# Kernel tuning notes

Measured on AMD Instinct MI355X. Metric: run time of the kernel, lower is better.

## Reference

```python
import jax, jax.numpy as jnp
import numpy as np

NHID = 512
NCLS = 250
CHUNK = 200  # words per class (equal class_chunks), vocab = NCLS*CHUNK = 50000
N = 2048     # flattened tokens (batch*seq after masking)


def setup_inputs() -> dict:
    key = jax.random.key(0)
    k1, k2, k3, k4, k5 = jax.random.split(key, 5)
    r = 0.1  # init_weights uniform range
    x = jax.random.normal(k1, (N, NHID), dtype=jnp.float32)
    cls_idx = jax.random.randint(k2, (N,), 0, NCLS, dtype=jnp.int64)
    Wc = jax.random.uniform(k3, (NCLS, NHID), jnp.float32, -r, r)   # cls_decoder.weight
    bc = jnp.zeros((NCLS,), jnp.float32)                             # cls_decoder.bias
    Ww = jax.random.uniform(k4, (NCLS, CHUNK, NHID), jnp.float32, -r, r)  # stacked words_decoders weights
    bw = jnp.zeros((NCLS, CHUNK), jnp.float32)                       # stacked words_decoders biases
    return {"x": x, "Wc": Wc, "bc": bc, "Ww": Ww, "bw": bw, "cls_idx": cls_idx}


def reference(x, Wc, bc, Ww, bw, cls_idx):
    # Class logits for every token: cls_decoder(input)
    p_class = jnp.einsum('nh,ch->nc', x, Wc) + bc          # [N, NCLS]
    # Per-class word decoders: each token goes through the Linear of its class.
    # Equivalent to the dict-based index_select + per-class Linear in the
    # original forward (rows reordered per-token instead of grouped by class).
    Wg = Ww[cls_idx]                                       # [N, CHUNK, NHID] irregular gather
    bg = bw[cls_idx]                                       # [N, CHUNK]
    p_words = jnp.einsum('nkh,nh->nk', Wg, x) + bg         # [N, CHUNK]
    # Concatenate class and within-class logits into one array output.
    return jnp.concatenate([p_class, p_words], axis=1)     # [N, NCLS+CHUNK]
```

## Files before the change

### kernel.cpp

```cpp
#include <hip/hip_runtime.h>

#define NHID   512
#define NCLS   250
#define CHUNK  200
#define NTOK   2048
#define NOUT   450
#define NBLK   500
#define NTHR   256
#define MAXTOK 64

typedef __attribute__((ext_vector_type(8))) short bf16x8;
typedef __attribute__((ext_vector_type(4))) float f32x4;

#define MFMA(a, b, c) __builtin_amdgcn_mfma_f32_16x16x32_bf16((a), (b), (c), 0, 0, 0)

__device__ __forceinline__ unsigned hpack(unsigned a, unsigned b) {
    return __builtin_amdgcn_perm(a, b, 0x07060302u);
}

__device__ __forceinline__ void cvt8(f32x4 va, f32x4 vb, bf16x8& h, bf16x8& l) {
    unsigned u0 = __float_as_uint(va[0]), u1 = __float_as_uint(va[1]);
    unsigned u2 = __float_as_uint(va[2]), u3 = __float_as_uint(va[3]);
    unsigned u4 = __float_as_uint(vb[0]), u5 = __float_as_uint(vb[1]);
    unsigned u6 = __float_as_uint(vb[2]), u7 = __float_as_uint(vb[3]);
    union { unsigned w[4]; bf16x8 v; } H, L;
    H.w[0] = hpack(u1, u0); H.w[1] = hpack(u3, u2);
    H.w[2] = hpack(u5, u4); H.w[3] = hpack(u7, u6);
    float r0 = va[0] - __uint_as_float(u0 & 0xffff0000u);
    float r1 = va[1] - __uint_as_float(u1 & 0xffff0000u);
    float r2 = va[2] - __uint_as_float(u2 & 0xffff0000u);
    float r3 = va[3] - __uint_as_float(u3 & 0xffff0000u);
    float r4 = vb[0] - __uint_as_float(u4 & 0xffff0000u);
    float r5 = vb[1] - __uint_as_float(u5 & 0xffff0000u);
    float r6 = vb[2] - __uint_as_float(u6 & 0xffff0000u);
    float r7 = vb[3] - __uint_as_float(u7 & 0xffff0000u);
    L.w[0] = hpack(__float_as_uint(r1), __float_as_uint(r0));
    L.w[1] = hpack(__float_as_uint(r3), __float_as_uint(r2));
    L.w[2] = hpack(__float_as_uint(r5), __float_as_uint(r4));
    L.w[3] = hpack(__float_as_uint(r7), __float_as_uint(r6));
    h = H.v; l = L.v;
}

#define WAITVM(nn) asm volatile("s_waitcnt vmcnt(" #nn ")" ::: "memory")
#define BL(k, off) asm volatile("global_load_dwordx4 %0, %1, off offset:%c2" \
        : "=v"(bv[k]) : "v"(wrow8), "i"(off))
#define BL2(s) BL(2*(s), (s)*128); BL(2*(s)+1, (s)*128 + 16)

#define KSTEP(s) { \
    const char* ab_ = (const char*)Afrag + n * 2048 + (s) * 128; \
    bf16x8 ah_ = *(const bf16x8*)(ab_ + (((q*2    ) ^ (n&7)) << 4)); \
    bf16x8 al_ = *(const bf16x8*)(ab_ + (((q*2 + 1) ^ (n&7)) << 4)); \
    bf16x8 bh_, bl_; cvt8(bv[2*(s)], bv[2*(s)+1], bh_, bl_); \
    acc = MFMA(ah_, bh_, acc); \
    acc = MFMA(al_, bh_, acc); \
    acc = MFMA(ah_, bl_, acc); }

__device__ __forceinline__ void class_unit(int u, int w8, int lane, int n, int q,
                                           const float* __restrict__ x,
                                           const float* __restrict__ Wc,
                                           const float* __restrict__ bc,
                                           float* __restrict__ out) {
    const int mt = u >> 1, hn = u & 1;
    const int g4 = (w8 >> 2) & 1, kk = w8 & 3;
    const int rC = (hn * 8 + g4 * 4 + kk) * 16 + n;
    const bool rv = rC < NCLS;
    const int  rc = rv ? rC : NCLS - 1;
    const float* ap = x  + (size_t)(mt * 16 + n) * NHID + q * 8;
    const float* bp = Wc + (size_t)rc * NHID + q * 8;
    const float bias = bc[rc];
    f32x4 acc = {0.f, 0.f, 0.f, 0.f};
    f32x4 qa[2][2], qb[2][2];
    #pragma unroll
    for (int j = 0; j < 2; ++j) {
        qa[j][0] = *(const f32x4*)(ap + j * 32);
        qa[j][1] = *(const f32x4*)(ap + j * 32 + 4);
        qb[j][0] = *(const f32x4*)(bp + j * 32);
        qb[j][1] = *(const f32x4*)(bp + j * 32 + 4);
    }
    #pragma unroll 2
    for (int s = 0; s < 16; ++s) {
        const int b = s & 1;
        bf16x8 ah, al, bh, bl;
        cvt8(qa[b][0], qa[b][1], ah, al);
        cvt8(qb[b][0], qb[b][1], bh, bl);
        acc = MFMA(ah, bh, acc);
        acc = MFMA(al, bh, acc);
        acc = MFMA(ah, bl, acc);
        if (s + 2 < 16) {
            qa[b][0] = *(const f32x4*)(ap + (s + 2) * 32);
            qa[b][1] = *(const f32x4*)(ap + (s + 2) * 32 + 4);
            qb[b][0] = *(const f32x4*)(bp + (s + 2) * 32);
            qb[b][1] = *(const f32x4*)(bp + (s + 2) * 32 + 4);
        }
    }
    if (rv) {
        #pragma unroll
        for (int i = 0; i < 4; ++i)
            out[(size_t)(mt * 16 + q * 4 + i) * NOUT + rc] = acc[i] + bias;
    }
}

__global__ __launch_bounds__(NTHR, 2)
void cbd_fused(const float* __restrict__ x,  const float* __restrict__ Wc,
               const float* __restrict__ bc, const float* __restrict__ Ww,
               const float* __restrict__ bw, const int* __restrict__ cls_idx,
               float* __restrict__ out)
{
    __shared__ short Afrag[16384];
    __shared__ int   toktmp[MAXTOK];

    const int tid  = threadIdx.x;
    const int wid  = tid >> 6;
    const int lane = tid & 63;
    const int n    = lane & 15;
    const int q    = lane >> 4;
    const int c    = blockIdx.x >> 1;
    const int h    = blockIdx.x & 1;

    int myvals[32];
    #pragma unroll
    for (int it = 0; it < 8; ++it) {
        int4 v = *(const int4*)&cls_idx[it * 256 + lane * 4];
        myvals[it*4+0] = v.x; myvals[it*4+1] = v.y;
        myvals[it*4+2] = v.z; myvals[it*4+3] = v.w;
    }
    int cnt = 0;
    #pragma unroll
    for (int j = 0; j < 32; ++j) {
        int idx  = (j >> 2) * 256 + lane * 4 + (j & 3);
        bool hit = (myvals[j] == c);
        unsigned long long m = __ballot(hit);
        if (hit) {
            int pos = cnt + (int)__popcll(m & ((1ull << lane) - 1ull));
            if (pos < MAXTOK) toktmp[pos] = idx;
        }
        cnt += (int)__popcll(m);
    }
    const int cnt1 = cnt < 16 ? cnt : 16;

    int tkS[4]; bool msk[4];
    if (cnt) {
        int mytokA = toktmp[n < cnt1 ? n : cnt1 - 1];
        #pragma unroll
        for (int i = 0; i < 4; ++i) {
            tkS[i] = __shfl(mytokA, q * 4 + i);
            msk[i] = (q * 4 + i) < cnt1;
        }
        #pragma unroll
        for (int rep = 0; rep < 4; ++rep) {
            int job = rep * 256 + tid;
            int tok = job >> 6, s = (job >> 2) & 15, qq = job & 3;
            int ti  = toktmp[tok < cnt1 ? tok : cnt1 - 1];
            const float* xp = x + (size_t)ti * NHID + s * 32 + qq * 8;
            f32x4 a0 = *(const f32x4*)xp, a1 = *(const f32x4*)(xp + 4);
            bf16x8 hh, ll; cvt8(a0, a1, hh, ll);
            char* ab = (char*)Afrag + tok * 2048 + s * 128;
            *(bf16x8*)(ab + (((qq * 2    ) ^ (tok & 7)) << 4)) = hh;
            *(bf16x8*)(ab + (((qq * 2 + 1) ^ (tok & 7)) << 4)) = ll;
        }
    }
    __syncthreads();

    if (cnt) {
        const int np = h ? 6 : 7;
        for (int pp = wid; pp < np; pp += 4) {
            const int P  = h * 7 + pp;
            const int r  = P * 16 + n;
            const int rr = r < CHUNK ? r : CHUNK - 1;
            const char* wrow8 =
                (const char*)(Ww + ((size_t)c * CHUNK + rr) * NHID + q * 8);
            float bias = bw[c * CHUNK + rr];

            WAITVM(0);
            __builtin_amdgcn_sched_barrier(0);

            f32x4 bv[32];
            BL2(0);  BL2(1);  BL2(2);  BL2(3);
            BL2(4);  BL2(5);  BL2(6);  BL2(7);
            BL2(8);  BL2(9);  BL2(10); BL2(11);
            BL2(12); BL2(13); BL2(14); BL2(15);

            f32x4 acc = {0.f, 0.f, 0.f, 0.f};
            WAITVM(24); __builtin_amdgcn_sched_barrier(0);
            KSTEP(0)  KSTEP(1)  KSTEP(2)  KSTEP(3)
            WAITVM(16); __builtin_amdgcn_sched_barrier(0);
            KSTEP(4)  KSTEP(5)  KSTEP(6)  KSTEP(7)
            WAITVM(8);  __builtin_amdgcn_sched_barrier(0);
            KSTEP(8)  KSTEP(9)  KSTEP(10) KSTEP(11)
            WAITVM(0);  __builtin_amdgcn_sched_barrier(0);
            KSTEP(12) KSTEP(13) KSTEP(14) KSTEP(15)

            if (r < CHUNK) {
                #pragma unroll
                for (int i = 0; i < 4; ++i)
                    if (msk[i])
                        out[(size_t)tkS[i] * NOUT + NCLS + r] = acc[i] + bias;
            }
        }
    }

    {
        int unit = -1;
        if (h == 0)          unit = c;
        else if (c < 6)      unit = NCLS + c;
        if (unit >= 0) {
            class_unit(unit, wid,     lane, n, q, x, Wc, bc, out);
            class_unit(unit, 4 + wid, lane, n, q, x, Wc, bc, out);
        }
    }

    if (h == 0 && cnt > 16) {
        const int cw = cnt < MAXTOK ? cnt : MAXTOK;
        const int ov = cw - 16;
        for (int j = tid; j < ov * CHUNK; j += NTHR) {
            const int g  = j / CHUNK;
            const int rr = j - g * CHUNK;
            const int ti = toktmp[16 + g];
            const float4* wr = (const float4*)(Ww + ((size_t)c * CHUNK + rr) * NHID);
            const float4* xr = (const float4*)(x + (size_t)ti * NHID);
            float s0 = 0.f, s1 = 0.f, s2 = 0.f, s3 = 0.f;
            #pragma unroll 4
            for (int k = 0; k < 128; ++k) {
                float4 a = wr[k], b = xr[k];
                s0 += a.x * b.x; s1 += a.y * b.y;
                s2 += a.z * b.z; s3 += a.w * b.w;
            }
            out[(size_t)ti * NOUT + NCLS + rr] =
                (s0 + s1) + (s2 + s3) + bw[c * CHUNK + rr];
        }
    }
}

extern "C" void kernel_launch(void* const* d_in, const int* in_sizes, int n_in,
                              void* d_out, int out_size, void* d_ws, size_t ws_size,
                              hipStream_t stream) {
    const float* x   = (const float*)d_in[0];
    const float* Wc  = (const float*)d_in[1];
    const float* bc  = (const float*)d_in[2];
    const float* Ww  = (const float*)d_in[3];
    const float* bw  = (const float*)d_in[4];
    const int*   cls = (const int*)d_in[5];
    float* out = (float*)d_out;
    hipLaunchKernelGGL(cbd_fused, dim3(NBLK), dim3(NTHR), 0, stream,
                       x, Wc, bc, Ww, bw, cls, out);
}
```

Baseline: 206.3 us.

## Split each class over four blocks with a rolling six-stage weight-load pipeline

Grid doubles to four blocks per class, so each wave handles at most one 16-row panel of the word decoder, and the fourth block's spare waves take a round-robin share of class-logit tiles. The full 32-register prefetch of weights is replaced by a six-stage rolling ring of loads with staggered vmcnt waits, and launch bounds rise to four blocks per CU. The aim is more parallelism and occupancy, with less register pressure, while the weight stream stays in flight. The cost is that every block redoes the cls_idx scan and x staging, and the work across blocks is uneven.

```diff
diff --git a/kernel.cpp b/kernel.cpp
--- a/kernel.cpp
+++ b/kernel.cpp
@@ -5,7 +5,7 @@
 #define CHUNK  200
 #define NTOK   2048
 #define NOUT   450
-#define NBLK   500
+#define NBLK   1000
 #define NTHR   256
 #define MAXTOK 64
 
@@ -41,16 +41,18 @@
     h = H.v; l = L.v;
 }
 
-#define WAITVM(nn) asm volatile("s_waitcnt vmcnt(" #nn ")" ::: "memory")
-#define BL(k, off) asm volatile("global_load_dwordx4 %0, %1, off offset:%c2" \
-        : "=v"(bv[k]) : "v"(wrow8), "i"(off))
-#define BL2(s) BL(2*(s), (s)*128); BL(2*(s)+1, (s)*128 + 16)
-
-#define KSTEP(s) { \
+#define WAITB(nn) do { asm volatile("s_waitcnt vmcnt(" #nn ")" ::: "memory"); \
+                       __builtin_amdgcn_sched_barrier(0); } while (0)
+#define ISSP(S, P) \
+    asm volatile("global_load_dwordx4 %0, %1, off offset:%c2" \
+        : "=v"(Q##S) : "v"(wrow8), "i"((P) * 128)); \
+    asm volatile("global_load_dwordx4 %0, %1, off offset:%c2" \
+        : "=v"(R##S) : "v"(wrow8), "i"((P) * 128 + 16));
+#define KST(S, s) { \
     const char* ab_ = (const char*)Afrag + n * 2048 + (s) * 128; \
     bf16x8 ah_ = *(const bf16x8*)(ab_ + (((q*2    ) ^ (n&7)) << 4)); \
     bf16x8 al_ = *(const bf16x8*)(ab_ + (((q*2 + 1) ^ (n&7)) << 4)); \
-    bf16x8 bh_, bl_; cvt8(bv[2*(s)], bv[2*(s)+1], bh_, bl_); \
+    bf16x8 bh_, bl_; cvt8(Q##S, R##S, bh_, bl_); \
     acc = MFMA(ah_, bh_, acc); \
     acc = MFMA(al_, bh_, acc); \
     acc = MFMA(ah_, bl_, acc); }
@@ -100,7 +102,7 @@
     }
 }
 
-__global__ __launch_bounds__(NTHR, 2)
+__global__ __launch_bounds__(NTHR, 4)
 void cbd_fused(const float* __restrict__ x,  const float* __restrict__ Wc,
                const float* __restrict__ bc, const float* __restrict__ Ww,
                const float* __restrict__ bw, const int* __restrict__ cls_idx,
@@ -114,8 +116,8 @@
     const int lane = tid & 63;
     const int n    = lane & 15;
     const int q    = lane >> 4;
-    const int c    = blockIdx.x >> 1;
-    const int h    = blockIdx.x & 1;
+    const int c    = blockIdx.x >> 2;
+    const int g    = blockIdx.x & 3;
 
     int myvals[32];
     #pragma unroll
@@ -161,61 +163,62 @@
     }
     __syncthreads();
 
-    if (cnt) {
-        const int np = h ? 6 : 7;
-        for (int pp = wid; pp < np; pp += 4) {
-            const int P  = h * 7 + pp;
-            const int r  = P * 16 + n;
-            const int rr = r < CHUNK ? r : CHUNK - 1;
-            const char* wrow8 =
-                (const char*)(Ww + ((size_t)c * CHUNK + rr) * NHID + q * 8);
-            float bias = bw[c * CHUNK + rr];
-
-            WAITVM(0);
-            __builtin_amdgcn_sched_barrier(0);
-
-            f32x4 bv[32];
-            BL2(0);  BL2(1);  BL2(2);  BL2(3);
-            BL2(4);  BL2(5);  BL2(6);  BL2(7);
-            BL2(8);  BL2(9);  BL2(10); BL2(11);
-            BL2(12); BL2(13); BL2(14); BL2(15);
-
-            f32x4 acc = {0.f, 0.f, 0.f, 0.f};
-            WAITVM(24); __builtin_amdgcn_sched_barrier(0);
-            KSTEP(0)  KSTEP(1)  KSTEP(2)  KSTEP(3)
-            WAITVM(16); __builtin_amdgcn_sched_barrier(0);
-            KSTEP(4)  KSTEP(5)  KSTEP(6)  KSTEP(7)
-            WAITVM(8);  __builtin_amdgcn_sched_barrier(0);
-            KSTEP(8)  KSTEP(9)  KSTEP(10) KSTEP(11)
-            WAITVM(0);  __builtin_amdgcn_sched_barrier(0);
-            KSTEP(12) KSTEP(13) KSTEP(14) KSTEP(15)
-
-            if (r < CHUNK) {
-                #pragma unroll
-                for (int i = 0; i < 4; ++i)
-                    if (msk[i])
-                        out[(size_t)tkS[i] * NOUT + NCLS + r] = acc[i] + bias;
-            }
-        }
-    }
-
-    {
-        int unit = -1;
-        if (h == 0)          unit = c;
-        else if (c < 6)      unit = NCLS + c;
-        if (unit >= 0) {
-            class_unit(unit, wid,     lane, n, q, x, Wc, bc, out);
-            class_unit(unit, 4 + wid, lane, n, q, x, Wc, bc, out);
-        }
-    }
-
-    if (h == 0 && cnt > 16) {
+    const int P = (g < 3) ? (g * 4 + wid) : 12;
+    if (cnt && (g < 3 || wid == 0)) {
+        const int r  = P * 16 + n;
+        const int rr = r < CHUNK ? r : CHUNK - 1;
+        const char* wrow8 =
+            (const char*)(Ww + ((size_t)c * CHUNK + rr) * NHID + q * 8);
+        float bias = bw[c * CHUNK + rr];
+
+        f32x4 Q0, Q1, Q2, Q3, Q4, Q5, R0, R1, R2, R3, R4, R5;
+        f32x4 acc = {0.f, 0.f, 0.f, 0.f};
+
+        WAITB(0);
+        ISSP(0, 0)  ISSP(1, 1)  ISSP(2, 2)  ISSP(3, 3)  ISSP(4, 4)  ISSP(5, 5)
+
+        WAITB(10); KST(0, 0)  ISSP(0, 6)
+        WAITB(10); KST(1, 1)  ISSP(1, 7)
+        WAITB(10); KST(2, 2)  ISSP(2, 8)
+        WAITB(10); KST(3, 3)  ISSP(3, 9)
+        WAITB(10); KST(4, 4)  ISSP(4, 10)
+        WAITB(10); KST(5, 5)  ISSP(5, 11)
+        WAITB(10); KST(0, 6)  ISSP(0, 12)
+        WAITB(10); KST(1, 7)  ISSP(1, 13)
+        WAITB(10); KST(2, 8)  ISSP(2, 14)
+        WAITB(10); KST(3, 9)  ISSP(3, 15)
+        WAITB(10); KST(4, 10)
+        WAITB(8);  KST(5, 11)
+        WAITB(6);  KST(0, 12)
+        WAITB(4);  KST(1, 13)
+        WAITB(2);  KST(2, 14)
+        WAITB(0);  KST(3, 15)
+
+        if (r < CHUNK) {
+            #pragma unroll
+            for (int i = 0; i < 4; ++i)
+                if (msk[i])
+                    out[(size_t)tkS[i] * NOUT + NCLS + r] = acc[i] + bias;
+        }
+    }
+
+    if (g == 3 && wid >= 1) {
+        const int base = (c * 3 + (wid - 1)) * 3;
+        #pragma unroll
+        for (int k = 0; k < 3; ++k) {
+            int t = base + k;
+            if (t < 2048)
+                class_unit(t >> 3, t & 7, lane, n, q, x, Wc, bc, out);
+        }
+    }
+
+    if (g == 3 && cnt > 16) {
         const int cw = cnt < MAXTOK ? cnt : MAXTOK;
         const int ov = cw - 16;
         for (int j = tid; j < ov * CHUNK; j += NTHR) {
-            const int g  = j / CHUNK;
-            const int rr = j - g * CHUNK;
-            const int ti = toktmp[16 + g];
+            const int gg = j / CHUNK;
+            const int rr = j - gg * CHUNK;
+            const int ti = toktmp[16 + gg];
             const float4* wr = (const float4*)(Ww + ((size_t)c * CHUNK + rr) * NHID);
             const float4* xr = (const float4*)(x + (size_t)ti * NHID);
             float s0 = 0.f, s1 = 0.f, s2 = 0.f, s3 = 0.f;
```

After: 209.3 us. No clear change (+1.5%).
